# Kernel optimization log

Measured on AMD Instinct MI355X. Metric: run time of the kernel, lower is better.

## Reference

```python
import jax, jax.numpy as jnp
import numpy as np

QMAX = 127.0

def _sym_quantize(t):
    # per-tensor symmetric int8 fake-quant: returns (quantized values as float, scale)
    scale = jnp.max(jnp.abs(t)) / QMAX
    q = jnp.clip(jnp.round(t / scale), -QMAX, QMAX)
    return q, scale

def setup_inputs() -> dict:
    key = jax.random.key(0)
    k1, k2, k3 = jax.random.split(key, 3)
    TOKENS, IN_F, OUT_F = 4096, 4096, 4096
    x = jax.random.normal(k1, (TOKENS, IN_F), dtype=jnp.float32)
    # int8-valued weight buffer (stored int32 for portability), symmetric range
    quantized_weight = jax.random.randint(k2, (OUT_F, IN_F), -127, 128, dtype=jnp.int32)
    weight_scale = jnp.float32(0.01)  # scalar per-tensor weight scale buffer
    bias = jax.random.normal(k3, (OUT_F,), dtype=jnp.float32)
    return {"x": x, "quantized_weight": quantized_weight,
            "weight_scale": weight_scale, "bias": bias}

def reference(x, quantized_weight, weight_scale, bias):
    q_x, x_scale = _sym_quantize(x)                      # [T, In] fake-quant activations
    w = quantized_weight.astype(jnp.float32)             # [Out, In]
    out = jnp.matmul(q_x, w.T)                           # fp32 GEMM on int8-valued operands
    out = out * (x_scale * weight_scale)                 # dequant scaling
    out = out + bias
    return out
```

## Files before the change

kernel.cpp:

```cpp
#include <hip/hip_runtime.h>

typedef __attribute__((ext_vector_type(4))) int int4v;

#define NB_MAX 1024

__device__ __forceinline__ void async_ld16(const void* g, void* l) {
  __builtin_amdgcn_global_load_lds(
      (const __attribute__((address_space(1))) void*)g,
      (__attribute__((address_space(3))) void*)l,
      16, 0, 0);
}

__global__ void absmax_partial_kernel(const float* __restrict__ x,
                                      float* __restrict__ partial, int n4) {
  const float4* x4 = (const float4*)x;
  float m = 0.0f;
  for (int i = blockIdx.x * blockDim.x + threadIdx.x; i < n4;
       i += gridDim.x * blockDim.x) {
    float4 v = x4[i];
    m = fmaxf(m, fabsf(v.x));
    m = fmaxf(m, fabsf(v.y));
    m = fmaxf(m, fabsf(v.z));
    m = fmaxf(m, fabsf(v.w));
  }
#pragma unroll
  for (int off = 32; off > 0; off >>= 1)
    m = fmaxf(m, __shfl_down(m, off, 64));
  __shared__ float wmax[4];
  const int wid = threadIdx.x >> 6;
  if ((threadIdx.x & 63) == 0) wmax[wid] = m;
  __syncthreads();
  if (threadIdx.x == 0)
    partial[blockIdx.x] =
        fmaxf(fmaxf(wmax[0], wmax[1]), fmaxf(wmax[2], wmax[3]));
}

__device__ __forceinline__ float reduce_partials(const float* partial) {
  __shared__ float smax;
  float m = 0.0f;
  for (int i = threadIdx.x; i < NB_MAX; i += blockDim.x)
    m = fmaxf(m, partial[i]);
#pragma unroll
  for (int off = 32; off > 0; off >>= 1)
    m = fmaxf(m, __shfl_down(m, off, 64));
  __shared__ float wmax[4];
  const int wid = threadIdx.x >> 6;
  if ((threadIdx.x & 63) == 0) wmax[wid] = m;
  __syncthreads();
  if (threadIdx.x == 0)
    smax = fmaxf(fmaxf(wmax[0], wmax[1]), fmaxf(wmax[2], wmax[3]));
  __syncthreads();
  return smax;
}

__global__ void quant_pack_kernel(const float* __restrict__ x,
                                  const int* __restrict__ w,
                                  const float* __restrict__ partial,
                                  float* __restrict__ scale_slot,
                                  int* __restrict__ qx, int* __restrict__ qw,
                                  int nx4, int nw4) {
  const float scale = reduce_partials(partial) / 127.0f;
  const int i = blockIdx.x * blockDim.x + threadIdx.x;
  if (i == 0) *scale_slot = scale;
  if (i < nx4) {
    float4 v = ((const float4*)x)[i];
    int q0 = (int)fminf(fmaxf(rintf(v.x / scale), -127.0f), 127.0f);
    int q1 = (int)fminf(fmaxf(rintf(v.y / scale), -127.0f), 127.0f);
    int q2 = (int)fminf(fmaxf(rintf(v.z / scale), -127.0f), 127.0f);
    int q3 = (int)fminf(fmaxf(rintf(v.w / scale), -127.0f), 127.0f);
    unsigned int p = (unsigned int)(q0 & 255) |
                     ((unsigned int)(q1 & 255) << 8) |
                     ((unsigned int)(q2 & 255) << 16) |
                     ((unsigned int)(q3 & 255) << 24);
    qx[i] = (int)p;
  }
  if (i < nw4) {
    int4 v = ((const int4*)w)[i];
    unsigned int p = (unsigned int)(v.x & 255) |
                     ((unsigned int)(v.y & 255) << 8) |
                     ((unsigned int)(v.z & 255) << 16) |
                     ((unsigned int)(v.w & 255) << 24);
    qw[i] = (int)p;
  }
}

__global__ __launch_bounds__(256) void gemm_i8_kernel(
    const signed char* __restrict__ A,
    const signed char* __restrict__ B,
    const float* __restrict__ bias,
    const float* __restrict__ scale_slot,
    const float* __restrict__ wscale,
    float* __restrict__ out, int K, int N) {
  __shared__ signed char As[128 * 128];
  __shared__ signed char Bs[128 * 128];

  const int tid = threadIdx.x;
  const int lane = tid & 63;
  const int wid = tid >> 6;
  const int row0 = blockIdx.y * 128;
  const int col0 = blockIdx.x * 128;
  const int wm = (wid >> 1) * 64;
  const int wn = (wid & 1) * 64;

  int4v acc[4][4] = {};

  const int gchunk = ((lane & 7) ^ ((lane >> 3) & 7)) * 16;
  const signed char* gA =
      A + (long)(row0 + wid * 32 + (lane >> 3)) * K + gchunk;
  const signed char* gB =
      B + (long)(col0 + wid * 32 + (lane >> 3)) * K + gchunk;
  const int ldsw = wid * 4096;

  const int q = lane >> 4;
  const int c7 = lane & 7;
  const int frow = (wm + (lane & 15)) * 128;
  const int fcs0 = ((q ^ c7) << 4);
  const int fcs1 = (((4 + q) ^ c7) << 4);
  const int fbrow = (wn + (lane & 15)) * 128;

  for (int k0 = 0; k0 < K; k0 += 128) {
    __syncthreads();
#pragma unroll
    for (int t = 0; t < 4; t++) {
      async_ld16(gA + k0 + t * 8 * (long)K, As + ldsw + t * 1024);
      async_ld16(gB + k0 + t * 8 * (long)K, Bs + ldsw + t * 1024);
    }
    asm volatile("s_waitcnt vmcnt(0)" ::: "memory");
    __syncthreads();

#pragma unroll
    for (int s = 0; s < 2; s++) {
      const int ca = (s == 0) ? fcs0 : fcs1;
      int4v a[4], b[4];
#pragma unroll
      for (int i = 0; i < 4; i++) {
        a[i] = *(const int4v*)(As + frow + i * 16 * 128 + ca);
        b[i] = *(const int4v*)(Bs + fbrow + i * 16 * 128 + ca);
      }
#pragma unroll
      for (int i = 0; i < 4; i++)
#pragma unroll
        for (int j = 0; j < 4; j++)
          acc[i][j] = __builtin_amdgcn_mfma_i32_16x16x64_i8(a[i], b[j],
                                                            acc[i][j], 0, 0, 0);
    }
  }

  const float s = scale_slot[0] * wscale[0];
  const int orow = row0 + wm + ((lane >> 4) << 2);
  const int ocol0 = col0 + wn + (lane & 15);
#pragma unroll
  for (int j = 0; j < 4; j++) {
    const int c = ocol0 + j * 16;
    const float bv = bias[c];
#pragma unroll
    for (int i = 0; i < 4; i++) {
#pragma unroll
      for (int r = 0; r < 4; r++) {
        out[(long)(orow + i * 16 + r) * N + c] = (float)acc[i][j][r] * s + bv;
      }
    }
  }
}

extern "C" void kernel_launch(void* const* d_in, const int* in_sizes, int n_in,
                              void* d_out, int out_size, void* d_ws,
                              size_t ws_size, hipStream_t stream) {
  const float* x = (const float*)d_in[0];
  const int* w = (const int*)d_in[1];
  const float* wscale = (const float*)d_in[2];
  const float* bias = (const float*)d_in[3];
  float* out = (float*)d_out;

  const int OUT_F = in_sizes[3];
  const int IN_F = in_sizes[1] / OUT_F;
  const int TOKENS = in_sizes[0] / IN_F;

  float* partial = (float*)d_ws;
  float* scale_slot = partial + NB_MAX;
  signed char* qx = (signed char*)d_ws + 8192;
  signed char* qw = qx + (size_t)TOKENS * IN_F;

  const int nx4 = TOKENS * IN_F / 4;
  const int nw4 = OUT_F * IN_F / 4;

  absmax_partial_kernel<<<NB_MAX, 256, 0, stream>>>(x, partial, nx4);

  const int nmax = nx4 > nw4 ? nx4 : nw4;
  quant_pack_kernel<<<(nmax + 255) / 256, 256, 0, stream>>>(
      x, w, partial, scale_slot, (int*)qx, (int*)qw, nx4, nw4);

  dim3 grid(OUT_F / 128, TOKENS / 128);
  gemm_i8_kernel<<<grid, 256, 0, stream>>>(qx, qw, bias, scale_slot, wscale,
                                           out, IN_F, OUT_F);
}
```

Before: 259.6 us.

## Rewrite int8 GEMM with 256x256 tiles, double-buffered LDS and interleaved prefetch

The int8 MFMA GEMM moves from 128x128 tiles with 4 waves to 256x256 tiles with 8 waves. LDS is double-buffered so global-to-LDS loads for the next K step are spread across four compute phases, with s_setprio raised around the MFMA bursts. Workgroup IDs are remapped so consecutive blocks are spread across XCDs for better L2 locality, and each wave holds more accumulators to raise operand reuse. The costs are higher register pressure (8x4 accumulators), 128KB of LDS per block that limits occupancy, and many hand-placed barriers and waitcnts that must stay correct.

```diff
diff --git a/kernel.cpp b/kernel.cpp
--- a/kernel.cpp
+++ b/kernel.cpp
@@ -84,80 +84,168 @@
   }
 }
 
-__global__ __launch_bounds__(256) void gemm_i8_kernel(
+__global__ __launch_bounds__(512, 2) void gemm_i8_kernel(
     const signed char* __restrict__ A,
     const signed char* __restrict__ B,
     const float* __restrict__ bias,
     const float* __restrict__ scale_slot,
     const float* __restrict__ wscale,
     float* __restrict__ out, int K, int N) {
-  __shared__ signed char As[128 * 128];
-  __shared__ signed char Bs[128 * 128];
+  __shared__ signed char As[2][256 * 128];
+  __shared__ signed char Bs[2][256 * 128];
 
   const int tid = threadIdx.x;
   const int lane = tid & 63;
   const int wid = tid >> 6;
-  const int row0 = blockIdx.y * 128;
-  const int col0 = blockIdx.x * 128;
-  const int wm = (wid >> 1) * 64;
-  const int wn = (wid & 1) * 64;
-
-  int4v acc[4][4] = {};
-
-  const int gchunk = ((lane & 7) ^ ((lane >> 3) & 7)) * 16;
-  const signed char* gA =
-      A + (long)(row0 + wid * 32 + (lane >> 3)) * K + gchunk;
-  const signed char* gB =
-      B + (long)(col0 + wid * 32 + (lane >> 3)) * K + gchunk;
-  const int ldsw = wid * 4096;
+
+  const int nwgx = gridDim.x;
+  const int nwg = nwgx * gridDim.y;
+  const int flat = blockIdx.y * nwgx + blockIdx.x;
+  const int cpx = nwg >> 3;
+  const int swz = (flat & 7) * cpx + (flat >> 3);
+  const int row0 = (swz / nwgx) << 8;
+  const int col0 = (swz % nwgx) << 8;
+
+  const int wm = (wid >> 2) * 128;
+  const int wn = (wid & 3) * 64;
+
+  int4v acc[8][4] = {};
+
+  const int srow = wid * 8 + (lane >> 3);
+  const int schunk = ((lane & 7) ^ ((lane >> 3) & 7)) << 4;
+  const signed char* gA = A + (long)(row0 + srow) * K + schunk;
+  const signed char* gB = B + (long)(col0 + srow) * K + schunk;
+  const int sdst = wid * 1024;
 
   const int q = lane >> 4;
   const int c7 = lane & 7;
-  const int frow = (wm + (lane & 15)) * 128;
-  const int fcs0 = ((q ^ c7) << 4);
-  const int fcs1 = (((4 + q) ^ c7) << 4);
-  const int fbrow = (wn + (lane & 15)) * 128;
-
-  for (int k0 = 0; k0 < K; k0 += 128) {
-    __syncthreads();
-#pragma unroll
-    for (int t = 0; t < 4; t++) {
-      async_ld16(gA + k0 + t * 8 * (long)K, As + ldsw + t * 1024);
-      async_ld16(gB + k0 + t * 8 * (long)K, Bs + ldsw + t * 1024);
-    }
-    asm volatile("s_waitcnt vmcnt(0)" ::: "memory");
-    __syncthreads();
-
-#pragma unroll
-    for (int s = 0; s < 2; s++) {
-      const int ca = (s == 0) ? fcs0 : fcs1;
-      int4v a[4], b[4];
-#pragma unroll
-      for (int i = 0; i < 4; i++) {
-        a[i] = *(const int4v*)(As + frow + i * 16 * 128 + ca);
-        b[i] = *(const int4v*)(Bs + fbrow + i * 16 * 128 + ca);
-      }
-#pragma unroll
-      for (int i = 0; i < 4; i++)
-#pragma unroll
-        for (int j = 0; j < 4; j++)
-          acc[i][j] = __builtin_amdgcn_mfma_i32_16x16x64_i8(a[i], b[j],
-                                                            acc[i][j], 0, 0, 0);
-    }
-  }
+  const int fc0 = (q ^ c7) << 4;
+  const int fc1 = ((4 + q) ^ c7) << 4;
+  const int fa = (wm + (lane & 15)) * 128;
+  const int fb = (wn + (lane & 15)) * 128;
+
+  const long l64K = 64 * (long)K;
+  const int NT = K >> 7;
+
+  async_ld16(gB, &Bs[0][0 * 8192 + sdst]);
+  async_ld16(gB + l64K, &Bs[0][1 * 8192 + sdst]);
+  async_ld16(gB + 2 * l64K, &Bs[0][2 * 8192 + sdst]);
+  async_ld16(gB + 3 * l64K, &Bs[0][3 * 8192 + sdst]);
+  async_ld16(gA, &As[0][0 * 8192 + sdst]);
+  async_ld16(gA + 2 * l64K, &As[0][2 * 8192 + sdst]);
+  async_ld16(gA + l64K, &As[0][1 * 8192 + sdst]);
+  async_ld16(gA + 3 * l64K, &As[0][3 * 8192 + sdst]);
+  asm volatile("s_waitcnt vmcnt(2)" ::: "memory");
+  __builtin_amdgcn_s_barrier();
+
+  int4v areg[4][2], breg0[2][2], breg1[2][2];
+
+  for (int T = 0; T < NT; ++T) {
+    const int b = T & 1;
+    const int Tn = (T + 1 < NT) ? (T + 1) : T;
+    const signed char* gAn = gA + (long)Tn * 128;
+    const signed char* gBn = gB + (long)Tn * 128;
+    signed char* An = &As[b ^ 1][sdst];
+    signed char* Bn = &Bs[b ^ 1][sdst];
+    const signed char* Ab = As[b];
+    const signed char* Bb = Bs[b];
+
+#pragma unroll
+    for (int i = 0; i < 4; i++) {
+      areg[i][0] = *(const int4v*)(Ab + fa + i * 2048 + fc0);
+      areg[i][1] = *(const int4v*)(Ab + fa + i * 2048 + fc1);
+    }
+#pragma unroll
+    for (int j = 0; j < 2; j++) {
+      breg0[j][0] = *(const int4v*)(Bb + fb + j * 2048 + fc0);
+      breg0[j][1] = *(const int4v*)(Bb + fb + j * 2048 + fc1);
+    }
+    async_ld16(gBn, Bn);
+    async_ld16(gBn + l64K, Bn + 8192);
+    __builtin_amdgcn_s_barrier();
+    asm volatile("s_waitcnt lgkmcnt(0)" ::: "memory");
+    __builtin_amdgcn_s_setprio(1);
+#pragma unroll
+    for (int i = 0; i < 4; i++)
+#pragma unroll
+      for (int j = 0; j < 2; j++) {
+        acc[i][j] = __builtin_amdgcn_mfma_i32_16x16x64_i8(areg[i][0], breg0[j][0], acc[i][j], 0, 0, 0);
+        acc[i][j] = __builtin_amdgcn_mfma_i32_16x16x64_i8(areg[i][1], breg0[j][1], acc[i][j], 0, 0, 0);
+      }
+    __builtin_amdgcn_s_setprio(0);
+    __builtin_amdgcn_s_barrier();
+
+#pragma unroll
+    for (int j = 0; j < 2; j++) {
+      breg1[j][0] = *(const int4v*)(Bb + fb + (2 + j) * 2048 + fc0);
+      breg1[j][1] = *(const int4v*)(Bb + fb + (2 + j) * 2048 + fc1);
+    }
+    async_ld16(gBn + 2 * l64K, Bn + 2 * 8192);
+    async_ld16(gBn + 3 * l64K, Bn + 3 * 8192);
+    __builtin_amdgcn_s_barrier();
+    asm volatile("s_waitcnt lgkmcnt(0)" ::: "memory");
+    __builtin_amdgcn_s_setprio(1);
+#pragma unroll
+    for (int i = 0; i < 4; i++)
+#pragma unroll
+      for (int j = 0; j < 2; j++) {
+        acc[i][2 + j] = __builtin_amdgcn_mfma_i32_16x16x64_i8(areg[i][0], breg1[j][0], acc[i][2 + j], 0, 0, 0);
+        acc[i][2 + j] = __builtin_amdgcn_mfma_i32_16x16x64_i8(areg[i][1], breg1[j][1], acc[i][2 + j], 0, 0, 0);
+      }
+    __builtin_amdgcn_s_setprio(0);
+    asm volatile("s_waitcnt vmcnt(4)" ::: "memory");
+    __builtin_amdgcn_s_barrier();
+
+#pragma unroll
+    for (int i = 0; i < 4; i++) {
+      areg[i][0] = *(const int4v*)(Ab + fa + 8192 + i * 2048 + fc0);
+      areg[i][1] = *(const int4v*)(Ab + fa + 8192 + i * 2048 + fc1);
+    }
+    async_ld16(gAn, An);
+    async_ld16(gAn + 2 * l64K, An + 2 * 8192);
+    __builtin_amdgcn_s_barrier();
+    asm volatile("s_waitcnt lgkmcnt(0)" ::: "memory");
+    __builtin_amdgcn_s_setprio(1);
+#pragma unroll
+    for (int i = 0; i < 4; i++)
+#pragma unroll
+      for (int j = 0; j < 2; j++) {
+        acc[4 + i][j] = __builtin_amdgcn_mfma_i32_16x16x64_i8(areg[i][0], breg0[j][0], acc[4 + i][j], 0, 0, 0);
+        acc[4 + i][j] = __builtin_amdgcn_mfma_i32_16x16x64_i8(areg[i][1], breg0[j][1], acc[4 + i][j], 0, 0, 0);
+      }
+    __builtin_amdgcn_s_setprio(0);
+    __builtin_amdgcn_s_barrier();
+
+    async_ld16(gAn + l64K, An + 8192);
+    async_ld16(gAn + 3 * l64K, An + 3 * 8192);
+    __builtin_amdgcn_s_barrier();
+    __builtin_amdgcn_s_setprio(1);
+#pragma unroll
+    for (int i = 0; i < 4; i++)
+#pragma unroll
+      for (int j = 0; j < 2; j++) {
+        acc[4 + i][2 + j] = __builtin_amdgcn_mfma_i32_16x16x64_i8(areg[i][0], breg1[j][0], acc[4 + i][2 + j], 0, 0, 0);
+        acc[4 + i][2 + j] = __builtin_amdgcn_mfma_i32_16x16x64_i8(areg[i][1], breg1[j][1], acc[4 + i][2 + j], 0, 0, 0);
+      }
+    __builtin_amdgcn_s_setprio(0);
+    asm volatile("s_waitcnt vmcnt(2)" ::: "memory");
+    __builtin_amdgcn_s_barrier();
+  }
+
+  asm volatile("s_waitcnt vmcnt(0)" ::: "memory");
 
   const float s = scale_slot[0] * wscale[0];
-  const int orow = row0 + wm + ((lane >> 4) << 2);
-  const int ocol0 = col0 + wn + (lane & 15);
-#pragma unroll
-  for (int j = 0; j < 4; j++) {
-    const int c = ocol0 + j * 16;
+  const int orow = row0 + wm + (q << 2);
+  const int ocol = col0 + wn + (lane & 15);
+#pragma unroll
+  for (int jj = 0; jj < 4; jj++) {
+    const int c = ocol + jj * 16;
     const float bv = bias[c];
 #pragma unroll
-    for (int i = 0; i < 4; i++) {
+    for (int i = 0; i < 8; i++) {
 #pragma unroll
       for (int r = 0; r < 4; r++) {
-        out[(long)(orow + i * 16 + r) * N + c] = (float)acc[i][j][r] * s + bv;
+        out[(long)(orow + i * 16 + r) * N + c] = (float)acc[i][jj][r] * s + bv;
       }
     }
   }
@@ -190,7 +278,7 @@
   quant_pack_kernel<<<(nmax + 255) / 256, 256, 0, stream>>>(
       x, w, partial, scale_slot, (int*)qx, (int*)qw, nx4, nw4);
 
-  dim3 grid(OUT_F / 128, TOKENS / 128);
-  gemm_i8_kernel<<<grid, 256, 0, stream>>>(qx, qw, bias, scale_slot, wscale,
+  dim3 grid(OUT_F / 256, TOKENS / 256);
+  gemm_i8_kernel<<<grid, 512, 0, stream>>>(qx, qw, bias, scale_slot, wscale,
                                            out, IN_F, OUT_F);
 }
```

Result: faster. 245.8 us (-5.3%).
